# Kernel optimization log

Hardware: AMD Instinct MI355X
Metric: run time of the kernel (lower is better)

## Reference

```python
import jax, jax.numpy as jnp
import numpy as np

WINDOW_SIZE = 11
SIGMA = 1.5

def _gaussian_window():
    x = np.arange(WINDOW_SIZE, dtype=np.float64) - WINDOW_SIZE // 2
    g = np.exp(-(x ** 2) / (2.0 * SIGMA ** 2))
    g = (g / g.sum()).astype(np.float32)
    w2 = np.outer(g, g)  # [11, 11]
    return jnp.asarray(w2)


def setup_inputs() -> dict:
    key = jax.random.key(0)
    k1, k2 = jax.random.split(key)
    B, C, H, W = 32, 3, 512, 512
    img1 = jax.random.uniform(k1, (B, C, H, W), dtype=jnp.float32)
    img2 = jax.random.uniform(k2, (B, C, H, W), dtype=jnp.float32)
    return {"img1": img1, "img2": img2}


def reference(img1, img2):
    # peak = 1.0, size_average = True
    c1 = jnp.float32(0.01 ** 2)
    c2 = jnp.float32(0.03 ** 2)
    C = img1.shape[1]
    w2 = _gaussian_window()

    # One fused depthwise conv over the 5 statistic planes (same math as 5
    # separate grouped convs in the original).
    stacked = jnp.concatenate(
        [img1, img2, img1 * img1, img2 * img2, img1 * img2], axis=1
    )  # [B, 5C, H, W]
    kernel = jnp.tile(w2[None, None], (5 * C, 1, 1, 1))  # [5C, 1, 11, 11]
    out = jax.lax.conv_general_dilated(
        stacked, kernel,
        window_strides=(1, 1), padding='VALID',
        feature_group_count=5 * C,
        dimension_numbers=('NCHW', 'OIHW', 'NCHW'),
    )  # [B, 5C, H-10, W-10]

    mu1 = out[:, 0 * C:1 * C]
    mu2 = out[:, 1 * C:2 * C]
    mu1_sq = mu1 * mu1
    mu2_sq = mu2 * mu2
    mu1_mu2 = mu1 * mu2
    sigma1_sq = out[:, 2 * C:3 * C] - mu1_sq
    sigma2_sq = out[:, 3 * C:4 * C] - mu2_sq
    sigma12 = out[:, 4 * C:5 * C] - mu1_mu2

    ssim_map = ((2 * mu1_mu2 + c1) * (2 * sigma12 + c2)) / (
        (mu1_sq + mu2_sq + c1) * (sigma1_sq + sigma2_sq + c2)
    )
    return jnp.mean(ssim_map)
```

## Files before the change

### kernel.cpp

```cpp
#include <hip/hip_runtime.h>


namespace {
constexpr int IMG_H = 512;
constexpr int IMG_W = 512;
constexpr int NIMG  = 96;
constexpr int OUT_H = 502;
constexpr int OUT_W = 502;
constexpr int RPB   = 64;
constexpr int QR    = 2;
constexpr int BUFW  = 544;
constexpr double TOTAL = 24192384.0;

constexpr double U0 = 0.0038659201;
constexpr double U1 = 0.0285655007;
constexpr double U2 = 0.1353352832366127;
constexpr double U3 = 0.4111122898;
constexpr double U4 = 0.8007374026;
constexpr double S  = 1.0 + 2.0 * (U0 + U1 + U2 + U3 + U4);
}

__device__ __forceinline__ float2 f2fma(float w, float2 a, float2 c) {
    return make_float2(fmaf(w, a.x, c.x), fmaf(w, a.y, c.y));
}

__global__ __launch_bounds__(256, 3) void ssim_main(const float* __restrict__ img1,
                                                    const float* __restrict__ img2,
                                                    double* __restrict__ acc)
{
    __shared__ __align__(16) float vrow[2][QR][4][BUFW];
    __shared__ float red[4];

    const float g[11] = {
        (float)(U0/S), (float)(U1/S), (float)(U2/S), (float)(U3/S), (float)(U4/S),
        (float)(1.0/S),
        (float)(U4/S), (float)(U3/S), (float)(U2/S), (float)(U1/S), (float)(U0/S)
    };
    constexpr float C1 = 1e-4f;
    constexpr float C2 = 9e-4f;

    const int t   = threadIdx.x;
    const int z   = blockIdx.y;
    const int oy0 = blockIdx.x * RPB;
    const int row_end = min(oy0 + RPB, OUT_H);

    const float2* p1 = (const float2*)(img1 + (size_t)z * (IMG_H * IMG_W)) + t;
    const float2* p2 = (const float2*)(img2 + (size_t)z * (IMG_H * IMG_W)) + t;

    const int c4w  = t >> 1;
    const int woff = ((c4w ^ ((c4w >> 3) & 7)) << 2) + ((t & 1) << 1);

    const int hq = t >> 7;
    const int cb = (t & 127) << 2;
    int roff[4];
    #pragma unroll
    for (int k = 0; k < 4; ++k) {
        int c4 = (cb >> 2) + k;
        roff[k] = (c4 ^ ((c4 >> 3) & 7)) << 2;
    }

    float local = 0.f;
    int p = 0;

    for (int r0 = oy0; r0 < row_end; r0 += QR, p ^= 1) {
        float2 am1[QR], am2[QR], app[QR], axy[QR];
        #pragma unroll
        for (int q = 0; q < QR; ++q) {
            am1[q] = make_float2(0.f, 0.f);
            am2[q] = make_float2(0.f, 0.f);
            app[q] = make_float2(0.f, 0.f);
            axy[q] = make_float2(0.f, 0.f);
        }
        #pragma unroll
        for (int j = 0; j < QR + 10; ++j) {
            const float2 x = p1[(r0 + j) * (IMG_W / 2)];
            const float2 y = p2[(r0 + j) * (IMG_W / 2)];
            const float2 pp = make_float2(fmaf(x.x, x.x, y.x * y.x),
                                          fmaf(x.y, x.y, y.y * y.y));
            const float2 xy = make_float2(x.x * y.x, x.y * y.y);
            #pragma unroll
            for (int q = 0; q < QR; ++q) {
                const int k = j - q;
                if (k >= 0 && k < 11) {
                    const float w = g[k];
                    am1[q] = f2fma(w, x,  am1[q]);
                    am2[q] = f2fma(w, y,  am2[q]);
                    app[q] = f2fma(w, pp, app[q]);
                    axy[q] = f2fma(w, xy, axy[q]);
                }
            }
        }
        #pragma unroll
        for (int q = 0; q < QR; ++q) {
            *(float2*)&vrow[p][q][0][woff] = am1[q];
            *(float2*)&vrow[p][q][1][woff] = am2[q];
            *(float2*)&vrow[p][q][2][woff] = app[q];
            *(float2*)&vrow[p][q][3][woff] = axy[q];
        }
        __syncthreads();

        const int rr = r0 + hq;
        if (rr < row_end) {
            float aa[4][4];
            #pragma unroll
            for (int ch = 0; ch < 4; ++ch) {
                const float* bc = &vrow[p][hq][ch][0];
                float f[16];
                #pragma unroll
                for (int k = 0; k < 4; ++k) {
                    float4 v = *(const float4*)(bc + roff[k]);
                    f[4*k+0] = v.x; f[4*k+1] = v.y; f[4*k+2] = v.z; f[4*k+3] = v.w;
                }
                #pragma unroll
                for (int j = 0; j < 4; ++j) {
                    float s = 0.f;
                    #pragma unroll
                    for (int k = 0; k < 11; ++k) s = fmaf(g[k], f[j + k], s);
                    aa[ch][j] = s;
                }
            }
            #pragma unroll
            for (int j = 0; j < 4; ++j) {
                if (cb + j < OUT_W) {
                    float mu1 = aa[0][j], mu2 = aa[1][j];
                    float ee  = aa[2][j], e12 = aa[3][j];
                    float mu11 = mu1 * mu1;
                    float mu22 = mu2 * mu2;
                    float mu12 = mu1 * mu2;
                    float mm   = mu11 + mu22;
                    float s12  = e12 - mu12;
                    float spp  = ee - mm;
                    float num = fmaf(2.f, mu12, C1) * fmaf(2.f, s12, C2);
                    float den = (mm + C1) * (spp + C2);
                    local = fmaf(num, __builtin_amdgcn_rcpf(den), local);
                }
            }
        }
    }

    #pragma unroll
    for (int off = 32; off > 0; off >>= 1) local += __shfl_down(local, off, 64);
    if ((t & 63) == 0) red[t >> 6] = local;
    __syncthreads();
    if (t == 0) {
        double s = (double)red[0] + (double)red[1] + (double)red[2] + (double)red[3];
        atomicAdd(acc, s);
    }
}

__global__ void ssim_fin(const double* __restrict__ acc, float* __restrict__ out)
{
    out[0] = (float)(acc[0] / TOTAL);
}

extern "C" void kernel_launch(void* const* d_in, const int* in_sizes, int n_in,
                              void* d_out, int out_size, void* d_ws, size_t ws_size,
                              hipStream_t stream)
{
    (void)in_sizes; (void)n_in; (void)out_size; (void)ws_size;
    const float* img1 = (const float*)d_in[0];
    const float* img2 = (const float*)d_in[1];
    double* acc = (double*)d_ws;

    hipMemsetAsync(d_ws, 0, sizeof(double), stream);
    dim3 grid((OUT_H + RPB - 1) / RPB, NIMG);
    hipLaunchKernelGGL(ssim_main, grid, dim3(256), 0, stream, img1, img2, acc);
    hipLaunchKernelGGL(ssim_fin, dim3(1), dim3(1), 0, stream, acc, (float*)d_out);
}
```

Measured before the change: 288.6 us.

## Keep a sliding register window of input rows and widen per-thread horizontal work

Input rows are now held in a register ring (wx/wy) that is shifted by QR rows each iteration, so each image row is loaded from global memory once per block instead of once per vertical output row group. QR goes from 2 to 4 and RPB from 64 to 48. The horizontal pass now has each thread compute 8 output columns instead of 4, which cuts redundant shared loads per output. The double-buffered shared memory becomes a single buffer guarded by an extra barrier. The costs are higher register pressure (launch bounds lowered to 2 blocks per SM), an added __syncthreads per iteration, and more halo overhead from the smaller row tiles.

```diff
diff --git a/kernel.cpp b/kernel.cpp
--- a/kernel.cpp
+++ b/kernel.cpp
@@ -7,8 +7,9 @@
 constexpr int NIMG  = 96;
 constexpr int OUT_H = 502;
 constexpr int OUT_W = 502;
-constexpr int RPB   = 64;
-constexpr int QR    = 2;
+constexpr int RPB   = 48;
+constexpr int QR    = 4;
+constexpr int WIN   = QR + 10;
 constexpr int BUFW  = 544;
 constexpr double TOTAL = 24192384.0;
 
@@ -24,11 +25,11 @@
     return make_float2(fmaf(w, a.x, c.x), fmaf(w, a.y, c.y));
 }
 
-__global__ __launch_bounds__(256, 3) void ssim_main(const float* __restrict__ img1,
+__global__ __launch_bounds__(256, 2) void ssim_main(const float* __restrict__ img1,
                                                     const float* __restrict__ img2,
                                                     double* __restrict__ acc)
 {
-    __shared__ __align__(16) float vrow[2][QR][4][BUFW];
+    __shared__ __align__(16) float vrow[QR][4][BUFW];
     __shared__ float red[4];
 
     const float g[11] = {
@@ -50,19 +51,32 @@
     const int c4w  = t >> 1;
     const int woff = ((c4w ^ ((c4w >> 3) & 7)) << 2) + ((t & 1) << 1);
 
-    const int hq = t >> 7;
-    const int cb = (t & 127) << 2;
-    int roff[4];
+    const int hq = t >> 6;
+    const int cb = (t & 63) << 3;
+    int roff[5];
     #pragma unroll
-    for (int k = 0; k < 4; ++k) {
+    for (int k = 0; k < 5; ++k) {
         int c4 = (cb >> 2) + k;
         roff[k] = (c4 ^ ((c4 >> 3) & 7)) << 2;
     }
 
+    float2 wx[WIN], wy[WIN];
+    #pragma unroll
+    for (int j = 0; j < WIN - QR; ++j) {
+        wx[j] = p1[(oy0 + j) * (IMG_W / 2)];
+        wy[j] = p2[(oy0 + j) * (IMG_W / 2)];
+    }
+
     float local = 0.f;
-    int p = 0;
 
-    for (int r0 = oy0; r0 < row_end; r0 += QR, p ^= 1) {
+    for (int r0 = oy0; r0 < row_end; r0 += QR) {
+        #pragma unroll
+        for (int i = 0; i < QR; ++i) {
+            const int row = min(r0 + (WIN - QR) + i, IMG_H - 1);
+            wx[WIN - QR + i] = p1[row * (IMG_W / 2)];
+            wy[WIN - QR + i] = p2[row * (IMG_W / 2)];
+        }
+
         float2 am1[QR], am2[QR], app[QR], axy[QR];
         #pragma unroll
         for (int q = 0; q < QR; ++q) {
@@ -72,9 +86,8 @@
             axy[q] = make_float2(0.f, 0.f);
         }
         #pragma unroll
-        for (int j = 0; j < QR + 10; ++j) {
-            const float2 x = p1[(r0 + j) * (IMG_W / 2)];
-            const float2 y = p2[(r0 + j) * (IMG_W / 2)];
+        for (int j = 0; j < WIN; ++j) {
+            const float2 x = wx[j], y = wy[j];
             const float2 pp = make_float2(fmaf(x.x, x.x, y.x * y.x),
                                           fmaf(x.y, x.y, y.y * y.y));
             const float2 xy = make_float2(x.x * y.x, x.y * y.y);
@@ -90,29 +103,33 @@
                 }
             }
         }
+        __syncthreads();
         #pragma unroll
         for (int q = 0; q < QR; ++q) {
-            *(float2*)&vrow[p][q][0][woff] = am1[q];
-            *(float2*)&vrow[p][q][1][woff] = am2[q];
-            *(float2*)&vrow[p][q][2][woff] = app[q];
-            *(float2*)&vrow[p][q][3][woff] = axy[q];
+            *(float2*)&vrow[q][0][woff] = am1[q];
+            *(float2*)&vrow[q][1][woff] = am2[q];
+            *(float2*)&vrow[q][2][woff] = app[q];
+            *(float2*)&vrow[q][3][woff] = axy[q];
         }
         __syncthreads();
 
+        #pragma unroll
+        for (int j = 0; j < WIN - QR; ++j) { wx[j] = wx[j + QR]; wy[j] = wy[j + QR]; }
+
         const int rr = r0 + hq;
         if (rr < row_end) {
-            float aa[4][4];
+            float aa[4][8];
             #pragma unroll
             for (int ch = 0; ch < 4; ++ch) {
-                const float* bc = &vrow[p][hq][ch][0];
-                float f[16];
+                const float* bc = &vrow[hq][ch][0];
+                float f[20];
                 #pragma unroll
-                for (int k = 0; k < 4; ++k) {
+                for (int k = 0; k < 5; ++k) {
                     float4 v = *(const float4*)(bc + roff[k]);
                     f[4*k+0] = v.x; f[4*k+1] = v.y; f[4*k+2] = v.z; f[4*k+3] = v.w;
                 }
                 #pragma unroll
-                for (int j = 0; j < 4; ++j) {
+                for (int j = 0; j < 8; ++j) {
                     float s = 0.f;
                     #pragma unroll
                     for (int k = 0; k < 11; ++k) s = fmaf(g[k], f[j + k], s);
@@ -120,7 +137,7 @@
                 }
             }
             #pragma unroll
-            for (int j = 0; j < 4; ++j) {
+            for (int j = 0; j < 8; ++j) {
                 if (cb + j < OUT_W) {
                     float mu1 = aa[0][j], mu2 = aa[1][j];
                     float ee  = aa[2][j], e12 = aa[3][j];
```

New measurement: 246.1 us. 1.17x faster.

## Replace LDS horizontal pass with per-wave full-row processing and lane shuffles

Applied to the files above, without the earlier changes.

Each wavefront now owns a 12-row chunk of one image, and each lane covers 8 contiguous columns of the full 512-wide row. The vertical Gaussian pass uses packed float2 FMAs on 16-byte loads. The horizontal pass takes neighbour-lane values through __shfl_down, so the shared-memory staging buffer and the per-iteration __syncthreads are gone. The cost is more accumulator registers (launch bounds lowered from 3 to 2 blocks per CU) and many cross-lane shuffles per row.

```diff
diff --git a/kernel.cpp b/kernel.cpp
--- a/kernel.cpp
+++ b/kernel.cpp
@@ -7,9 +7,10 @@
 constexpr int NIMG  = 96;
 constexpr int OUT_H = 502;
 constexpr int OUT_W = 502;
-constexpr int RPB   = 64;
-constexpr int QR    = 2;
-constexpr int BUFW  = 544;
+constexpr int RPW   = 12;
+constexpr int CHUNKS = (OUT_H + RPW - 1) / RPW;
+constexpr int NWAVES = NIMG * CHUNKS;
+constexpr int HW    = IMG_H * IMG_W;
 constexpr double TOTAL = 24192384.0;
 
 constexpr double U0 = 0.0038659201;
@@ -20,15 +21,18 @@
 constexpr double S  = 1.0 + 2.0 * (U0 + U1 + U2 + U3 + U4);
 }
 
-__device__ __forceinline__ float2 f2fma(float w, float2 a, float2 c) {
-    return make_float2(fmaf(w, a.x, c.x), fmaf(w, a.y, c.y));
+typedef float vf2 __attribute__((ext_vector_type(2)));
+typedef float vf4 __attribute__((ext_vector_type(4)));
+
+__device__ __forceinline__ vf2 pk_fma(float w, vf2 a, vf2 c) {
+    vf2 wv = {w, w};
+    return __builtin_elementwise_fma(wv, a, c);
 }
 
-__global__ __launch_bounds__(256, 3) void ssim_main(const float* __restrict__ img1,
+__global__ __launch_bounds__(256, 2) void ssim_main(const float* __restrict__ img1,
                                                     const float* __restrict__ img2,
                                                     double* __restrict__ acc)
 {
-    __shared__ __align__(16) float vrow[2][QR][4][BUFW];
     __shared__ float red[4];
 
     const float g[11] = {
@@ -39,100 +43,106 @@
     constexpr float C1 = 1e-4f;
     constexpr float C2 = 9e-4f;
 
-    const int t   = threadIdx.x;
-    const int z   = blockIdx.y;
-    const int oy0 = blockIdx.x * RPB;
-    const int row_end = min(oy0 + RPB, OUT_H);
+    const int t    = threadIdx.x;
+    const int lane = t & 63;
+    const int wv   = t >> 6;
+    const int gw   = blockIdx.x * 4 + wv;
+    const int z     = gw / CHUNKS;
+    const int chunk = gw - z * CHUNKS;
+    const int r0b   = chunk * RPW;
+    const int row_end = min(r0b + RPW, OUT_H);
 
-    const float2* p1 = (const float2*)(img1 + (size_t)z * (IMG_H * IMG_W)) + t;
-    const float2* p2 = (const float2*)(img2 + (size_t)z * (IMG_H * IMG_W)) + t;
-
-    const int c4w  = t >> 1;
-    const int woff = ((c4w ^ ((c4w >> 3) & 7)) << 2) + ((t & 1) << 1);
-
-    const int hq = t >> 7;
-    const int cb = (t & 127) << 2;
-    int roff[4];
-    #pragma unroll
-    for (int k = 0; k < 4; ++k) {
-        int c4 = (cb >> 2) + k;
-        roff[k] = (c4 ^ ((c4 >> 3) & 7)) << 2;
-    }
+    const float* b1 = img1 + (size_t)z * HW + lane * 8;
+    const float* b2 = img2 + (size_t)z * HW + lane * 8;
 
     float local = 0.f;
-    int p = 0;
 
-    for (int r0 = oy0; r0 < row_end; r0 += QR, p ^= 1) {
-        float2 am1[QR], am2[QR], app[QR], axy[QR];
+    for (int r0 = r0b; r0 < row_end; r0 += 2) {
+        vf2 a_[4][2][4];
         #pragma unroll
-        for (int q = 0; q < QR; ++q) {
-            am1[q] = make_float2(0.f, 0.f);
-            am2[q] = make_float2(0.f, 0.f);
-            app[q] = make_float2(0.f, 0.f);
-            axy[q] = make_float2(0.f, 0.f);
-        }
+        for (int ch = 0; ch < 4; ++ch)
+            #pragma unroll
+            for (int q = 0; q < 2; ++q)
+                #pragma unroll
+                for (int i = 0; i < 4; ++i) a_[ch][q][i] = (vf2){0.f, 0.f};
+
         #pragma unroll
-        for (int j = 0; j < QR + 10; ++j) {
-            const float2 x = p1[(r0 + j) * (IMG_W / 2)];
-            const float2 y = p2[(r0 + j) * (IMG_W / 2)];
-            const float2 pp = make_float2(fmaf(x.x, x.x, y.x * y.x),
-                                          fmaf(x.y, x.y, y.y * y.y));
-            const float2 xy = make_float2(x.x * y.x, x.y * y.y);
+        for (int j = 0; j < 12; ++j) {
+            const float* r1 = b1 + (r0 + j) * IMG_W;
+            const float* r2 = b2 + (r0 + j) * IMG_W;
+            const vf4 xlo = *(const vf4*)r1;
+            const vf4 xhi = *(const vf4*)(r1 + 4);
+            const vf4 ylo = *(const vf4*)r2;
+            const vf4 yhi = *(const vf4*)(r2 + 4);
+            vf2 xs[4] = {xlo.xy, xlo.zw, xhi.xy, xhi.zw};
+            vf2 ys[4] = {ylo.xy, ylo.zw, yhi.xy, yhi.zw};
+            vf2 pp[4], xy[4];
             #pragma unroll
-            for (int q = 0; q < QR; ++q) {
+            for (int i = 0; i < 4; ++i) {
+                pp[i] = __builtin_elementwise_fma(ys[i], ys[i], xs[i] * xs[i]);
+                xy[i] = xs[i] * ys[i];
+            }
+            #pragma unroll
+            for (int q = 0; q < 2; ++q) {
                 const int k = j - q;
                 if (k >= 0 && k < 11) {
                     const float w = g[k];
-                    am1[q] = f2fma(w, x,  am1[q]);
-                    am2[q] = f2fma(w, y,  am2[q]);
-                    app[q] = f2fma(w, pp, app[q]);
-                    axy[q] = f2fma(w, xy, axy[q]);
+                    #pragma unroll
+                    for (int i = 0; i < 4; ++i) {
+                        a_[0][q][i] = pk_fma(w, xs[i], a_[0][q][i]);
+                        a_[1][q][i] = pk_fma(w, ys[i], a_[1][q][i]);
+                        a_[2][q][i] = pk_fma(w, pp[i], a_[2][q][i]);
+                        a_[3][q][i] = pk_fma(w, xy[i], a_[3][q][i]);
+                    }
                 }
             }
         }
+
         #pragma unroll
-        for (int q = 0; q < QR; ++q) {
-            *(float2*)&vrow[p][q][0][woff] = am1[q];
-            *(float2*)&vrow[p][q][1][woff] = am2[q];
-            *(float2*)&vrow[p][q][2][woff] = app[q];
-            *(float2*)&vrow[p][q][3][woff] = axy[q];
-        }
-        __syncthreads();
-
-        const int rr = r0 + hq;
-        if (rr < row_end) {
-            float aa[4][4];
-            #pragma unroll
-            for (int ch = 0; ch < 4; ++ch) {
-                const float* bc = &vrow[p][hq][ch][0];
-                float f[16];
+        for (int q = 0; q < 2; ++q) {
+            if (r0 + q < row_end) {
+                float hh[4][8];
                 #pragma unroll
-                for (int k = 0; k < 4; ++k) {
-                    float4 v = *(const float4*)(bc + roff[k]);
-                    f[4*k+0] = v.x; f[4*k+1] = v.y; f[4*k+2] = v.z; f[4*k+3] = v.w;
+                for (int ch = 0; ch < 4; ++ch) {
+                    const vf2 a0 = a_[ch][q][0], a1 = a_[ch][q][1];
+                    const vf2 a2 = a_[ch][q][2], a3 = a_[ch][q][3];
+                    float f[18];
+                    f[0]  = a0.x; f[1]  = a0.y; f[2]  = a1.x; f[3]  = a1.y;
+                    f[4]  = a2.x; f[5]  = a2.y; f[6]  = a3.x; f[7]  = a3.y;
+                    f[8]  = __shfl_down(a0.x, 1, 64);
+                    f[9]  = __shfl_down(a0.y, 1, 64);
+                    f[10] = __shfl_down(a1.x, 1, 64);
+                    f[11] = __shfl_down(a1.y, 1, 64);
+                    f[12] = __shfl_down(a2.x, 1, 64);
+                    f[13] = __shfl_down(a2.y, 1, 64);
+                    f[14] = __shfl_down(a3.x, 1, 64);
+                    f[15] = __shfl_down(a3.y, 1, 64);
+                    f[16] = __shfl_down(a0.x, 2, 64);
+                    f[17] = __shfl_down(a0.y, 2, 64);
+                    #pragma unroll
+                    for (int o = 0; o < 8; ++o) {
+                        float s = 0.f;
+                        #pragma unroll
+                        for (int k = 0; k < 11; ++k) s = fmaf(g[k], f[o + k], s);
+                        hh[ch][o] = s;
+                    }
                 }
                 #pragma unroll
-                for (int j = 0; j < 4; ++j) {
-                    float s = 0.f;
-                    #pragma unroll
-                    for (int k = 0; k < 11; ++k) s = fmaf(g[k], f[j + k], s);
-                    aa[ch][j] = s;
-                }
-            }
-            #pragma unroll
-            for (int j = 0; j < 4; ++j) {
-                if (cb + j < OUT_W) {
-                    float mu1 = aa[0][j], mu2 = aa[1][j];
-                    float ee  = aa[2][j], e12 = aa[3][j];
-                    float mu11 = mu1 * mu1;
-                    float mu22 = mu2 * mu2;
-                    float mu12 = mu1 * mu2;
-                    float mm   = mu11 + mu22;
-                    float s12  = e12 - mu12;
-                    float spp  = ee - mm;
-                    float num = fmaf(2.f, mu12, C1) * fmaf(2.f, s12, C2);
-                    float den = (mm + C1) * (spp + C2);
-                    local = fmaf(num, __builtin_amdgcn_rcpf(den), local);
+                for (int o = 0; o < 8; ++o) {
+                    const int col = lane * 8 + o;
+                    if (col < OUT_W) {
+                        const float mu1 = hh[0][o], mu2 = hh[1][o];
+                        const float ee  = hh[2][o], e12 = hh[3][o];
+                        const float mu11 = mu1 * mu1;
+                        const float mu22 = mu2 * mu2;
+                        const float mu12 = mu1 * mu2;
+                        const float mm   = mu11 + mu22;
+                        const float s12  = e12 - mu12;
+                        const float spp  = ee - mm;
+                        const float num = fmaf(2.f, mu12, C1) * fmaf(2.f, s12, C2);
+                        const float den = (mm + C1) * (spp + C2);
+                        local = fmaf(num, __builtin_amdgcn_rcpf(den), local);
+                    }
                 }
             }
         }
@@ -140,7 +150,7 @@
 
     #pragma unroll
     for (int off = 32; off > 0; off >>= 1) local += __shfl_down(local, off, 64);
-    if ((t & 63) == 0) red[t >> 6] = local;
+    if (lane == 0) red[wv] = local;
     __syncthreads();
     if (t == 0) {
         double s = (double)red[0] + (double)red[1] + (double)red[2] + (double)red[3];
@@ -163,7 +173,7 @@
     double* acc = (double*)d_ws;
 
     hipMemsetAsync(d_ws, 0, sizeof(double), stream);
-    dim3 grid((OUT_H + RPB - 1) / RPB, NIMG);
-    hipLaunchKernelGGL(ssim_main, grid, dim3(256), 0, stream, img1, img2, acc);
+    hipLaunchKernelGGL(ssim_main, dim3(NWAVES / 4), dim3(256), 0, stream,
+                       img1, img2, acc);
     hipLaunchKernelGGL(ssim_fin, dim3(1), dim3(1), 0, stream, acc, (float*)d_out);
 }
```

New measurement: 725.1 us. 2.51x slower.
